# Performance work log

Measured on AMD Instinct MI355X. Metric: run time of the kernel, lower is better.

Reference implementation:

```python
import jax, jax.numpy as jnp
import numpy as np

D_MODEL = 1024
D_INNER = 2048
N_EXPERTS = 8
TOP_K = 2
INIT_STD = 0.02


def setup_inputs() -> dict:
    key = jax.random.key(0)
    ks = jax.random.split(key, 6)
    B, S = 2, 2048
    x = jax.random.normal(ks[0], (B, S, D_MODEL), dtype=jnp.float32)
    router_w = jax.random.normal(ks[1], (N_EXPERTS, D_MODEL), dtype=jnp.float32) * (INIT_STD * 0.1)
    router_b = jnp.zeros((N_EXPERTS,), dtype=jnp.float32)
    gate_w = jax.random.normal(ks[2], (N_EXPERTS, D_MODEL, D_INNER), dtype=jnp.float32) * INIT_STD
    up_w = jax.random.normal(ks[3], (N_EXPERTS, D_MODEL, D_INNER), dtype=jnp.float32) * INIT_STD
    down_w = jax.random.normal(ks[4], (N_EXPERTS, D_INNER, D_MODEL), dtype=jnp.float32) * INIT_STD
    return {"x": x, "router_w": router_w, "router_b": router_b,
            "gate_w": gate_w, "up_w": up_w, "down_w": down_w}


def reference(x, router_w, router_b, gate_w, up_w, down_w):
    # Router: softmax over experts, top-k, renormalize top-k probs.
    logits = jnp.einsum('bsd,ed->bse', x, router_w) + router_b          # [B,S,E]
    probs = jax.nn.softmax(logits, axis=-1)
    top_p, top_i = jax.lax.top_k(probs, TOP_K)                           # [B,S,K]
    top_p = top_p / jnp.sum(top_p, axis=-1, keepdims=True)
    # Per-expert combine weight: c[b,s,e] = sum_k top_p[b,s,k] * [top_i[b,s,k]==e]
    onehot = jax.nn.one_hot(top_i, N_EXPERTS, dtype=x.dtype)             # [B,S,K,E]
    combine = jnp.einsum('bsk,bske->bse', top_p, onehot)                 # [B,S,E]
    # SwiGLU FFN for every expert (dense form of the masked dispatch),
    # zeroed/weighted by combine coefficients.
    g = jnp.einsum('bsd,edf->ebsf', x, gate_w)                           # [E,B,S,F]
    u = jnp.einsum('bsd,edf->ebsf', x, up_w)
    h = jax.nn.silu(g) * u
    y = jnp.einsum('ebsf,efd->ebsd', h, down_w)                          # [E,B,S,D]
    out = jnp.einsum('ebsd,bse->bsd', y, combine)
    return out
```

## Files before the change

kernel.cpp:

```cpp
#include <hip/hip_runtime.h>
#include <hip/hip_bf16.h>
#include <stdint.h>

#define D_MODEL 1024
#define D_INNER 2048
#define NEXP 8
#define TOPK 2
#define T256 40
#define T128 72

typedef float f32x4 __attribute__((ext_vector_type(4)));
typedef short bf16x8 __attribute__((ext_vector_type(8)));

#define MEMFENCE asm volatile("" ::: "memory")

__device__ __forceinline__ unsigned short f2b(float f) {
    union { float f; uint32_t u; } v; v.f = f;
    uint32_t u = v.u;
    return (unsigned short)((u + 0x7fffu + ((u >> 16) & 1u)) >> 16);
}

__device__ __forceinline__ void gl_lds16(const void* g, void* l) {
    __builtin_amdgcn_global_load_lds((const __attribute__((address_space(1))) void*)g,
                                     (__attribute__((address_space(3))) void*)l, 16, 0, 0);
}

__global__ __launch_bounds__(256) void tcast3_kernel(
    const float* __restrict__ gw, const float* __restrict__ uw, const float* __restrict__ dw,
    unsigned short* __restrict__ gT, unsigned short* __restrict__ uT, unsigned short* __restrict__ dT)
{
    __shared__ unsigned short S[64][68];
    int which = blockIdx.z >> 3;
    int e = blockIdx.z & 7;
    const float* in; unsigned short* out; int K, N;
    if (which == 0)      { in = gw; out = gT; K = D_MODEL; N = D_INNER; }
    else if (which == 1) { in = uw; out = uT; K = D_MODEL; N = D_INNER; }
    else                 { in = dw; out = dT; K = D_INNER; N = D_MODEL; }
    int n0 = blockIdx.x * 64, k0 = blockIdx.y * 64;
    if (n0 >= N || k0 >= K) return;
    const float* ib = in + (size_t)e * K * N;
    unsigned short* ob = out + (size_t)e * N * K;
    int tid = threadIdx.x;
    int kk = tid >> 4, nn4 = (tid & 15) * 4;
#pragma unroll
    for (int j = 0; j < 4; j++) {
        int k = kk + 16 * j;
        float4 v = *(const float4*)&ib[(size_t)(k0 + k) * N + n0 + nn4];
        ushort4 s; s.x = f2b(v.x); s.y = f2b(v.y); s.z = f2b(v.z); s.w = f2b(v.w);
        *(ushort4*)&S[k][nn4] = s;
    }
    __syncthreads();
    int nn = tid >> 4, kk4 = (tid & 15) * 4;
#pragma unroll
    for (int j = 0; j < 4; j++) {
        int n = nn + 16 * j;
        ushort4 s;
        s.x = S[kk4 + 0][n]; s.y = S[kk4 + 1][n];
        s.z = S[kk4 + 2][n]; s.w = S[kk4 + 3][n];
        *(ushort4*)&ob[(size_t)(n0 + n) * K + k0 + kk4] = s;
    }
}

__global__ __launch_bounds__(64) void router_kernel(
    const float* __restrict__ x, const float* __restrict__ rw,
    const float* __restrict__ rb, unsigned short* __restrict__ xb,
    int* __restrict__ top_i, float* __restrict__ top_w, int T)
{
    int t = blockIdx.x;
    if (t >= T) return;
    int l = threadIdx.x;
    float xv[16];
#pragma unroll
    for (int i = 0; i < 16; i++) xv[i] = x[(size_t)t * D_MODEL + l + 64 * i];
#pragma unroll
    for (int i = 0; i < 16; i++) xb[(size_t)t * D_MODEL + l + 64 * i] = f2b(xv[i]);
    float logit[NEXP];
#pragma unroll
    for (int e = 0; e < NEXP; e++) {
        float acc = 0.f;
#pragma unroll
        for (int i = 0; i < 16; i++) acc += xv[i] * rw[e * D_MODEL + l + 64 * i];
#pragma unroll
        for (int s = 32; s > 0; s >>= 1) acc += __shfl_xor(acc, s, 64);
        logit[e] = acc + rb[e];
    }
    if (l == 0) {
        int i0 = 0; float m0 = logit[0];
#pragma unroll
        for (int e = 1; e < NEXP; e++) if (logit[e] > m0) { m0 = logit[e]; i0 = e; }
        int i1 = -1; float m1 = -3.0e38f;
#pragma unroll
        for (int e = 0; e < NEXP; e++) {
            if (e == i0) continue;
            if (logit[e] > m1) { m1 = logit[e]; i1 = e; }
        }
        float w0 = 1.f / (1.f + expf(m1 - m0));
        top_i[t * 2 + 0] = i0; top_i[t * 2 + 1] = i1;
        top_w[t * 2 + 0] = w0; top_w[t * 2 + 1] = 1.f - w0;
    }
}

__global__ __launch_bounds__(256) void bucket_kernel(
    const int* __restrict__ top_i, const float* __restrict__ top_w,
    int* __restrict__ meta, int* __restrict__ tok_of_slot,
    float* __restrict__ w_of_slot, int T)
{
    __shared__ int cnt[256][NEXP];
    __shared__ int pre[256][NEXP];
    __shared__ int tot[NEXP];
    __shared__ int off[NEXP + 1];
    int tid = threadIdx.x;
    int per = (T + 255) / 256;
    int t0 = tid * per;
    for (int e = 0; e < NEXP; e++) cnt[tid][e] = 0;
    for (int t = t0; t < t0 + per && t < T; t++)
        for (int k = 0; k < TOPK; k++) cnt[tid][top_i[t * 2 + k]]++;
    __syncthreads();
    if (tid < NEXP) {
        int run = 0;
        for (int i = 0; i < 256; i++) { pre[i][tid] = run; run += cnt[i][tid]; }
        tot[tid] = run;
    }
    __syncthreads();
    if (tid == 0) {
        off[0] = 0;
        for (int e = 0; e < NEXP; e++) off[e + 1] = off[e] + tot[e];
        for (int e = 0; e <= NEXP; e++) meta[e] = off[e];
        int nt = 0;
        for (int e = 0; e < NEXP; e++)
            for (int r = off[e]; r < off[e + 1]; r += 256)
                meta[16 + nt++] = (e << 16) | r;
        for (; nt < T256; nt++) meta[16 + nt] = -1;
        nt = 0;
        for (int e = 0; e < NEXP; e++)
            for (int r = off[e]; r < off[e + 1]; r += 128)
                meta[64 + nt++] = (e << 16) | r;
        for (; nt < T128; nt++) meta[64 + nt] = -1;
    }
    __syncthreads();
    int lc[NEXP];
#pragma unroll
    for (int e = 0; e < NEXP; e++) lc[e] = 0;
    for (int t = t0; t < t0 + per && t < T; t++) {
        for (int k = 0; k < TOPK; k++) {
            int e = top_i[t * 2 + k];
            int slot = off[e] + pre[tid][e] + lc[e]++;
            tok_of_slot[slot] = t;
            w_of_slot[slot] = top_w[t * 2 + k];
        }
    }
}

__global__ __launch_bounds__(512, 2) void moe_gate_up(
    const unsigned short* __restrict__ xb, const unsigned short* __restrict__ wgT,
    const unsigned short* __restrict__ wuT, const int* __restrict__ meta,
    const int* __restrict__ tok_of_slot, unsigned short* __restrict__ H)
{
    extern __shared__ __align__(16) unsigned short lds[];

    int lin = blockIdx.x;
    int strip = (lin & 7) * 2 + ((lin >> 3) & 1);
    int tix = lin >> 4;
    int packed = meta[16 + tix];
    if (packed < 0) return;
    int e = packed >> 16, row0 = packed & 0xffff;
    int Mloc = min(256, meta[e + 1] - row0);
    int f0 = strip * 128;

    int tid = threadIdx.x, wv = tid >> 6, lane = tid & 63;
    int c = tid & 7, rr = tid >> 3;

    const unsigned short* srcA[4];
    const unsigned short* srcG[2];
    const unsigned short* srcU[2];
#pragma unroll
    for (int j = 0; j < 4; j++) {
        int row = j * 64 + rr;
        int slot = row0 + ((row < Mloc) ? row : 0);
        srcA[j] = xb + (size_t)tok_of_slot[slot] * D_MODEL + 8 * (c ^ (row & 7));
    }
#pragma unroll
    for (int j = 0; j < 2; j++) {
        int row = j * 64 + rr;
        size_t wb = (size_t)e * D_MODEL * D_INNER + (size_t)(f0 + row) * D_MODEL + 8 * (c ^ (row & 7));
        srcG[j] = wgT + wb; srcU[j] = wuT + wb;
    }

    int wm = wv >> 1, wn = wv & 1;
    int lrow = lane & 15, kgrp = lane >> 4;
    int sw = lrow & 7;
    int co0 = 8 * (kgrp ^ sw);
    int co1 = 8 * ((4 + kgrp) ^ sw);

    int arow[4], brow[4];
#pragma unroll
    for (int i = 0; i < 4; i++) arow[i] = (wm * 64 + i * 16 + lrow) * 64;
#pragma unroll
    for (int i = 0; i < 4; i++) brow[i] = (wn * 64 + i * 16 + lrow) * 64;

    f32x4 accg[4][4], accu[4][4];
#pragma unroll
    for (int i = 0; i < 4; i++)
#pragma unroll
        for (int j = 0; j < 4; j++) {
            accg[i][j] = (f32x4){0.f, 0.f, 0.f, 0.f};
            accu[i][j] = (f32x4){0.f, 0.f, 0.f, 0.f};
        }

    auto stage = [&](int u) {
        int kk = u * 64;
        unsigned short* base = lds + (u & 1) * 32768;
#pragma unroll
        for (int j = 0; j < 4; j++)
            gl_lds16(srcA[j] + kk, base + (j * 512 + wv * 64) * 8);
#pragma unroll
        for (int j = 0; j < 2; j++) {
            gl_lds16(srcG[j] + kk, base + 16384 + (j * 512 + wv * 64) * 8);
            gl_lds16(srcU[j] + kk, base + 24576 + (j * 512 + wv * 64) * 8);
        }
    };

    bf16x8 a[4], bg[4], bu[4];
    auto load_frags = [&](int u, int co) {
        const unsigned short* base = lds + (u & 1) * 32768;
#pragma unroll
        for (int i = 0; i < 4; i++) a[i] = *(const bf16x8*)(base + arow[i] + co);
#pragma unroll
        for (int i = 0; i < 4; i++) bg[i] = *(const bf16x8*)(base + 16384 + brow[i] + co);
#pragma unroll
        for (int i = 0; i < 4; i++) bu[i] = *(const bf16x8*)(base + 24576 + brow[i] + co);
    };

    const int NT = D_MODEL / 64;
    stage(0);
    MEMFENCE;
    asm volatile("s_waitcnt vmcnt(0)" ::: "memory");
    __builtin_amdgcn_s_barrier();
    MEMFENCE;
    load_frags(0, co0);

    for (int t = 0; t < NT; ++t) {
        if (t + 1 < NT) stage(t + 1);
        __builtin_amdgcn_sched_barrier(0);
        __builtin_amdgcn_s_setprio(1);
#pragma unroll
        for (int fm = 0; fm < 4; fm++)
#pragma unroll
            for (int fn = 0; fn < 4; fn++) {
                accg[fm][fn] = __builtin_amdgcn_mfma_f32_16x16x32_bf16(a[fm], bg[fn], accg[fm][fn], 0, 0, 0);
                accu[fm][fn] = __builtin_amdgcn_mfma_f32_16x16x32_bf16(a[fm], bu[fn], accu[fm][fn], 0, 0, 0);
            }
        __builtin_amdgcn_s_setprio(0);
        load_frags(t, co1);
        __builtin_amdgcn_s_setprio(1);
#pragma unroll
        for (int fm = 0; fm < 4; fm++)
#pragma unroll
            for (int fn = 0; fn < 4; fn++) {
                accg[fm][fn] = __builtin_amdgcn_mfma_f32_16x16x32_bf16(a[fm], bg[fn], accg[fm][fn], 0, 0, 0);
                accu[fm][fn] = __builtin_amdgcn_mfma_f32_16x16x32_bf16(a[fm], bu[fn], accu[fm][fn], 0, 0, 0);
            }
        __builtin_amdgcn_s_setprio(0);
        __builtin_amdgcn_sched_barrier(0);
        asm volatile("s_waitcnt vmcnt(0)" ::: "memory");
        __builtin_amdgcn_s_barrier();
        MEMFENCE;
        if (t + 1 < NT) load_frags(t + 1, co0);
    }

#pragma unroll
    for (int fm = 0; fm < 4; fm++)
#pragma unroll
        for (int fn = 0; fn < 4; fn++)
#pragma unroll
            for (int r = 0; r < 4; r++) {
                int m = wm * 64 + fm * 16 + kgrp * 4 + r;
                if (m < Mloc) {
                    int n = wn * 64 + fn * 16 + lrow;
                    float g = accg[fm][fn][r], u = accu[fm][fn][r];
                    float h = g / (1.f + __expf(-g)) * u;
                    H[(size_t)(row0 + m) * D_INNER + f0 + n] = f2b(h);
                }
            }
}

__global__ __launch_bounds__(512, 2) void moe_down(
    const unsigned short* __restrict__ H, const unsigned short* __restrict__ wdT,
    const int* __restrict__ meta, const int* __restrict__ tok_of_slot,
    const float* __restrict__ w_of_slot, float* __restrict__ out, int S2)
{
    extern __shared__ __align__(16) unsigned short lds[];
    __shared__ int toks[128];
    __shared__ float wts[128];

    int lin = blockIdx.x;
    int d0 = (lin & 3) * 256;
    int tix = lin >> 2;
    int packed = meta[64 + tix];
    if (packed < 0) return;
    int e = packed >> 16, row0 = packed & 0xffff;
    int Mloc = min(128, meta[e + 1] - row0);

    int tid = threadIdx.x, wv = tid >> 6, lane = tid & 63;
    if (tid < 128) {
        bool v = tid < Mloc;
        toks[tid] = v ? tok_of_slot[row0 + tid] : 0;
        wts[tid] = v ? w_of_slot[row0 + tid] : 0.f;
    }
    int c = tid & 7, rr = tid >> 3;

    const unsigned short* srcA[2];
    const unsigned short* srcB[4];
#pragma unroll
    for (int j = 0; j < 2; j++) {
        int row = j * 64 + rr;
        int slot = min(row0 + row, S2 - 1);
        srcA[j] = H + (size_t)slot * D_INNER + 8 * (c ^ (row & 7));
    }
#pragma unroll
    for (int j = 0; j < 4; j++) {
        int row = j * 64 + rr;
        srcB[j] = wdT + (size_t)e * D_INNER * D_MODEL + (size_t)(d0 + row) * D_INNER + 8 * (c ^ (row & 7));
    }

    int wm = wv >> 2, wn = wv & 3;
    int lrow = lane & 15, kgrp = lane >> 4;
    int sw = lrow & 7;
    int co0 = 8 * (kgrp ^ sw);
    int co1 = 8 * ((4 + kgrp) ^ sw);

    int arow[4], brow[4];
#pragma unroll
    for (int i = 0; i < 4; i++) arow[i] = (wm * 64 + i * 16 + lrow) * 64;
#pragma unroll
    for (int i = 0; i < 4; i++) brow[i] = 8192 + (wn * 64 + i * 16 + lrow) * 64;

    f32x4 acc[4][4];
#pragma unroll
    for (int i = 0; i < 4; i++)
#pragma unroll
        for (int j = 0; j < 4; j++) acc[i][j] = (f32x4){0.f, 0.f, 0.f, 0.f};

    auto stage = [&](int u) {
        int kk = u * 64;
        unsigned short* base = lds + (u & 1) * 24576;
#pragma unroll
        for (int j = 0; j < 2; j++)
            gl_lds16(srcA[j] + kk, base + (j * 512 + wv * 64) * 8);
#pragma unroll
        for (int j = 0; j < 4; j++)
            gl_lds16(srcB[j] + kk, base + 8192 + (j * 512 + wv * 64) * 8);
    };

    bf16x8 a[4], b[4];
    auto load_frags = [&](int u, int co) {
        const unsigned short* base = lds + (u & 1) * 24576;
#pragma unroll
        for (int i = 0; i < 4; i++) a[i] = *(const bf16x8*)(base + arow[i] + co);
#pragma unroll
        for (int i = 0; i < 4; i++) b[i] = *(const bf16x8*)(base + brow[i] + co);
    };

    const int NT = D_INNER / 64;
    stage(0);
    MEMFENCE;
    asm volatile("s_waitcnt vmcnt(0)" ::: "memory");
    __builtin_amdgcn_s_barrier();
    MEMFENCE;
    load_frags(0, co0);

    for (int t = 0; t < NT; ++t) {
        if (t + 1 < NT) stage(t + 1);
        __builtin_amdgcn_sched_barrier(0);
        __builtin_amdgcn_s_setprio(1);
#pragma unroll
        for (int fm = 0; fm < 4; fm++)
#pragma unroll
            for (int fn = 0; fn < 4; fn++)
                acc[fm][fn] = __builtin_amdgcn_mfma_f32_16x16x32_bf16(a[fm], b[fn], acc[fm][fn], 0, 0, 0);
        __builtin_amdgcn_s_setprio(0);
        load_frags(t, co1);
        __builtin_amdgcn_s_setprio(1);
#pragma unroll
        for (int fm = 0; fm < 4; fm++)
#pragma unroll
            for (int fn = 0; fn < 4; fn++)
                acc[fm][fn] = __builtin_amdgcn_mfma_f32_16x16x32_bf16(a[fm], b[fn], acc[fm][fn], 0, 0, 0);
        __builtin_amdgcn_s_setprio(0);
        __builtin_amdgcn_sched_barrier(0);
        asm volatile("s_waitcnt vmcnt(0)" ::: "memory");
        __builtin_amdgcn_s_barrier();
        MEMFENCE;
        if (t + 1 < NT) load_frags(t + 1, co0);
    }

#pragma unroll
    for (int fm = 0; fm < 4; fm++)
#pragma unroll
        for (int fn = 0; fn < 4; fn++)
#pragma unroll
            for (int r = 0; r < 4; r++) {
                int m = wm * 64 + fm * 16 + kgrp * 4 + r;
                if (m < Mloc) {
                    int n = wn * 64 + fn * 16 + lrow;
                    atomicAdd(&out[(size_t)toks[m] * D_MODEL + d0 + n], wts[m] * acc[fm][fn][r]);
                }
            }
}

extern "C" void kernel_launch(void* const* d_in, const int* in_sizes, int n_in,
                              void* d_out, int out_size, void* d_ws, size_t ws_size,
                              hipStream_t stream) {
    const float* x  = (const float*)d_in[0];
    const float* rw = (const float*)d_in[1];
    const float* rb = (const float*)d_in[2];
    const float* gw = (const float*)d_in[3];
    const float* uw = (const float*)d_in[4];
    const float* dw = (const float*)d_in[5];
    float* out = (float*)d_out;

    int T = in_sizes[0] / D_MODEL;
    int S2 = 2 * T;

    char* ws = (char*)d_ws;
    size_t cur = 0;
    auto take = [&](size_t bytes) { char* p = ws + cur; cur = (cur + bytes + 255) & ~(size_t)255; return p; };
    int*   top_i = (int*)take((size_t)S2 * 4);
    float* top_w = (float*)take((size_t)S2 * 4);
    int*   meta  = (int*)take(1024);
    int*   tos   = (int*)take((size_t)S2 * 4);
    float* wos   = (float*)take((size_t)S2 * 4);
    unsigned short* xb  = (unsigned short*)take((size_t)T * D_MODEL * 2);
    unsigned short* wgT = (unsigned short*)take((size_t)NEXP * D_MODEL * D_INNER * 2);
    unsigned short* wuT = (unsigned short*)take((size_t)NEXP * D_MODEL * D_INNER * 2);
    unsigned short* wdT = (unsigned short*)take((size_t)NEXP * D_MODEL * D_INNER * 2);
    unsigned short* H   = (unsigned short*)take((size_t)S2 * D_INNER * 2);

    static const int GU_LDS = 2 * 32768 * 2;
    static const int DN_LDS = 2 * 24576 * 2;
    hipFuncSetAttribute((const void*)moe_gate_up,
                        hipFuncAttributeMaxDynamicSharedMemorySize, GU_LDS);
    hipFuncSetAttribute((const void*)moe_down,
                        hipFuncAttributeMaxDynamicSharedMemorySize, DN_LDS);

    hipMemsetAsync(d_out, 0, (size_t)out_size * sizeof(float), stream);

    tcast3_kernel<<<dim3(32, 32, 24), 256, 0, stream>>>(gw, uw, dw, wgT, wuT, wdT);
    router_kernel<<<T, 64, 0, stream>>>(x, rw, rb, xb, top_i, top_w, T);
    bucket_kernel<<<1, 256, 0, stream>>>(top_i, top_w, meta, tos, wos, T);

    moe_gate_up<<<T256 * 16, 512, GU_LDS, stream>>>(xb, wgT, wuT, meta, tos, H);
    moe_down<<<T128 * 4, 512, DN_LDS, stream>>>(H, wdT, meta, tos, wos, out, S2);
}
```

Before: 269.8 us.

## Shrink MoE GEMM tiles to 128-row blocks with 3-stage LDS ring pipeline

Both expert GEMM kernels move from 512-thread blocks with 256x128 or 128x256 tiles and a double-buffered 64-wide K step to 256-thread blocks with 128x64 or 128x128 tiles, a 32-wide K step and a triple-buffered LDS ring that keeps two stages in flight via partial vmcnt waits. In gate/up, separate waves now compute gate and up, and the SwiGLU is combined through an LDS exchange. The intent is more blocks and more resident blocks per CU, plus better overlap of global loads, on a grid that is otherwise small and imbalanced. In exchange, each tile reuses data less, so global traffic per FLOP rises, and there are more barriers per unit of K.

```diff
diff --git a/kernel.cpp b/kernel.cpp
--- a/kernel.cpp
+++ b/kernel.cpp
@@ -13,6 +13,12 @@
 typedef short bf16x8 __attribute__((ext_vector_type(8)));
 
 #define MEMFENCE asm volatile("" ::: "memory")
+#define SB __builtin_amdgcn_sched_barrier(0)
+#define LGKM0 asm volatile("s_waitcnt lgkmcnt(0)" ::: "memory")
+#define VM0 asm volatile("s_waitcnt vmcnt(0)" ::: "memory")
+#define VM4 asm volatile("s_waitcnt vmcnt(4)" ::: "memory")
+#define BAR __builtin_amdgcn_s_barrier()
+#define SW2(r) (((r) >> 1) & 3)
 
 __device__ __forceinline__ unsigned short f2b(float f) {
     union { float f; uint32_t u; } v; v.f = f;
@@ -130,11 +136,13 @@
         for (int e = 0; e < NEXP; e++)
             for (int r = off[e]; r < off[e + 1]; r += 256)
                 meta[16 + nt++] = (e << 16) | r;
+        meta[11] = nt;
         for (; nt < T256; nt++) meta[16 + nt] = -1;
         nt = 0;
         for (int e = 0; e < NEXP; e++)
             for (int r = off[e]; r < off[e + 1]; r += 128)
                 meta[64 + nt++] = (e << 16) | r;
+        meta[12] = nt;
         for (; nt < T128; nt++) meta[64 + nt] = -1;
     }
     __syncthreads();
@@ -151,7 +159,7 @@
     }
 }
 
-__global__ __launch_bounds__(512, 2) void moe_gate_up(
+__global__ __launch_bounds__(256, 3) void moe_gate_up(
     const unsigned short* __restrict__ xb, const unsigned short* __restrict__ wgT,
     const unsigned short* __restrict__ wuT, const int* __restrict__ meta,
     const int* __restrict__ tok_of_slot, unsigned short* __restrict__ H)
@@ -159,132 +167,125 @@
     extern __shared__ __align__(16) unsigned short lds[];
 
     int lin = blockIdx.x;
-    int strip = (lin & 7) * 2 + ((lin >> 3) & 1);
-    int tix = lin >> 4;
-    int packed = meta[16 + tix];
+    int strip = (lin & 7) * 4 + ((lin >> 3) & 3);
+    int tix = lin >> 5;
+    int packed = meta[64 + tix];
     if (packed < 0) return;
     int e = packed >> 16, row0 = packed & 0xffff;
-    int Mloc = min(256, meta[e + 1] - row0);
-    int f0 = strip * 128;
+    int Mloc = min(128, meta[e + 1] - row0);
+    int f0 = strip * 64;
 
     int tid = threadIdx.x, wv = tid >> 6, lane = tid & 63;
-    int c = tid & 7, rr = tid >> 3;
-
-    const unsigned short* srcA[4];
-    const unsigned short* srcG[2];
-    const unsigned short* srcU[2];
-#pragma unroll
-    for (int j = 0; j < 4; j++) {
-        int row = j * 64 + rr;
-        int slot = row0 + ((row < Mloc) ? row : 0);
-        srcA[j] = xb + (size_t)tok_of_slot[slot] * D_MODEL + 8 * (c ^ (row & 7));
-    }
+    int lrow = lane & 15, kgrp = lane >> 4;
+    int sel = wv & 1, wm = wv >> 1;
+    int co = 8 * (kgrp ^ SW2(lrow));
+
+    const unsigned short* sA[2];
+    int dA[2];
 #pragma unroll
     for (int j = 0; j < 2; j++) {
-        int row = j * 64 + rr;
-        size_t wb = (size_t)e * D_MODEL * D_INNER + (size_t)(f0 + row) * D_MODEL + 8 * (c ^ (row & 7));
-        srcG[j] = wgT + wb; srcU[j] = wuT + wb;
-    }
-
-    int wm = wv >> 1, wn = wv & 1;
-    int lrow = lane & 15, kgrp = lane >> 4;
-    int sw = lrow & 7;
-    int co0 = 8 * (kgrp ^ sw);
-    int co1 = 8 * ((4 + kgrp) ^ sw);
-
-    int arow[4], brow[4];
-#pragma unroll
-    for (int i = 0; i < 4; i++) arow[i] = (wm * 64 + i * 16 + lrow) * 64;
-#pragma unroll
-    for (int i = 0; i < 4; i++) brow[i] = (wn * 64 + i * 16 + lrow) * 64;
-
-    f32x4 accg[4][4], accu[4][4];
+        int idx = j * 256 + tid;
+        int r = idx >> 2, c = idx & 3;
+        int slot = row0 + ((r < Mloc) ? r : 0);
+        sA[j] = xb + (size_t)tok_of_slot[slot] * D_MODEL + 8 * (c ^ SW2(r));
+        dA[j] = idx * 8;
+    }
+    const unsigned short *sG, *sU;
+    {
+        int r = tid >> 2, c = tid & 3;
+        size_t wb = (size_t)e * D_MODEL * D_INNER + (size_t)(f0 + r) * D_MODEL + 8 * (c ^ SW2(r));
+        sG = wgT + wb; sU = wuT + wb;
+    }
+
+    int aoff[4], boff[4];
+#pragma unroll
+    for (int i = 0; i < 4; i++) aoff[i] = (wm * 64 + i * 16 + lrow) * 32 + co;
+    int bb = sel ? 6144 : 4096;
+#pragma unroll
+    for (int i = 0; i < 4; i++) boff[i] = bb + (i * 16 + lrow) * 32 + co;
+
+    f32x4 acc[4][4];
 #pragma unroll
     for (int i = 0; i < 4; i++)
 #pragma unroll
-        for (int j = 0; j < 4; j++) {
-            accg[i][j] = (f32x4){0.f, 0.f, 0.f, 0.f};
-            accu[i][j] = (f32x4){0.f, 0.f, 0.f, 0.f};
-        }
+        for (int j = 0; j < 4; j++) acc[i][j] = (f32x4){0.f, 0.f, 0.f, 0.f};
 
     auto stage = [&](int u) {
-        int kk = u * 64;
-        unsigned short* base = lds + (u & 1) * 32768;
-#pragma unroll
-        for (int j = 0; j < 4; j++)
-            gl_lds16(srcA[j] + kk, base + (j * 512 + wv * 64) * 8);
-#pragma unroll
-        for (int j = 0; j < 2; j++) {
-            gl_lds16(srcG[j] + kk, base + 16384 + (j * 512 + wv * 64) * 8);
-            gl_lds16(srcU[j] + kk, base + 24576 + (j * 512 + wv * 64) * 8);
-        }
+        int kk = u * 32;
+        unsigned short* b = lds + (u % 3) * 8192;
+        gl_lds16(sA[0] + kk, b + dA[0]);
+        gl_lds16(sA[1] + kk, b + dA[1]);
+        gl_lds16(sG + kk, b + 4096 + tid * 8);
+        gl_lds16(sU + kk, b + 6144 + tid * 8);
     };
 
-    bf16x8 a[4], bg[4], bu[4];
-    auto load_frags = [&](int u, int co) {
-        const unsigned short* base = lds + (u & 1) * 32768;
-#pragma unroll
-        for (int i = 0; i < 4; i++) a[i] = *(const bf16x8*)(base + arow[i] + co);
-#pragma unroll
-        for (int i = 0; i < 4; i++) bg[i] = *(const bf16x8*)(base + 16384 + brow[i] + co);
-#pragma unroll
-        for (int i = 0; i < 4; i++) bu[i] = *(const bf16x8*)(base + 24576 + brow[i] + co);
+    bf16x8 a[4], bfr[4];
+    auto load_frags = [&](int u) {
+        const unsigned short* b = lds + (u % 3) * 8192;
+#pragma unroll
+        for (int i = 0; i < 4; i++) a[i] = *(const bf16x8*)(b + aoff[i]);
+#pragma unroll
+        for (int i = 0; i < 4; i++) bfr[i] = *(const bf16x8*)(b + boff[i]);
     };
 
-    const int NT = D_MODEL / 64;
-    stage(0);
+    const int NT = D_MODEL / 32;
+    stage(0); stage(1);
     MEMFENCE;
-    asm volatile("s_waitcnt vmcnt(0)" ::: "memory");
-    __builtin_amdgcn_s_barrier();
-    MEMFENCE;
-    load_frags(0, co0);
+    VM4;
+    BAR; MEMFENCE;
+    load_frags(0);
 
     for (int t = 0; t < NT; ++t) {
-        if (t + 1 < NT) stage(t + 1);
-        __builtin_amdgcn_sched_barrier(0);
+        if (t + 2 < NT) stage(t + 2);
+        SB;
         __builtin_amdgcn_s_setprio(1);
 #pragma unroll
-        for (int fm = 0; fm < 4; fm++)
-#pragma unroll
-            for (int fn = 0; fn < 4; fn++) {
-                accg[fm][fn] = __builtin_amdgcn_mfma_f32_16x16x32_bf16(a[fm], bg[fn], accg[fm][fn], 0, 0, 0);
-                accu[fm][fn] = __builtin_amdgcn_mfma_f32_16x16x32_bf16(a[fm], bu[fn], accu[fm][fn], 0, 0, 0);
-            }
+        for (int i = 0; i < 4; i++)
+#pragma unroll
+            for (int j = 0; j < 4; j++)
+                acc[i][j] = __builtin_amdgcn_mfma_f32_16x16x32_bf16(a[i], bfr[j], acc[i][j], 0, 0, 0);
         __builtin_amdgcn_s_setprio(0);
-        load_frags(t, co1);
-        __builtin_amdgcn_s_setprio(1);
-#pragma unroll
-        for (int fm = 0; fm < 4; fm++)
-#pragma unroll
-            for (int fn = 0; fn < 4; fn++) {
-                accg[fm][fn] = __builtin_amdgcn_mfma_f32_16x16x32_bf16(a[fm], bg[fn], accg[fm][fn], 0, 0, 0);
-                accu[fm][fn] = __builtin_amdgcn_mfma_f32_16x16x32_bf16(a[fm], bu[fn], accu[fm][fn], 0, 0, 0);
-            }
-        __builtin_amdgcn_s_setprio(0);
-        __builtin_amdgcn_sched_barrier(0);
-        asm volatile("s_waitcnt vmcnt(0)" ::: "memory");
-        __builtin_amdgcn_s_barrier();
-        MEMFENCE;
-        if (t + 1 < NT) load_frags(t + 1, co0);
-    }
-
-#pragma unroll
-    for (int fm = 0; fm < 4; fm++)
-#pragma unroll
-        for (int fn = 0; fn < 4; fn++)
-#pragma unroll
-            for (int r = 0; r < 4; r++) {
-                int m = wm * 64 + fm * 16 + kgrp * 4 + r;
-                if (m < Mloc) {
-                    int n = wn * 64 + fn * 16 + lrow;
-                    float g = accg[fm][fn][r], u = accu[fm][fn][r];
-                    float h = g / (1.f + __expf(-g)) * u;
-                    H[(size_t)(row0 + m) * D_INNER + f0 + n] = f2b(h);
+        SB;
+        LGKM0;
+        if (t + 2 < NT) { VM4; } else { VM0; }
+        BAR; MEMFENCE;
+        if (t + 1 < NT) load_frags(t + 1);
+    }
+
+    __syncthreads();
+    float* ex = (float*)lds;
+    if (sel == 1) {
+        float* dst = ex + wm * 4160;
+#pragma unroll
+        for (int i = 0; i < 4; i++)
+#pragma unroll
+            for (int j = 0; j < 4; j++)
+#pragma unroll
+                for (int r = 0; r < 4; r++)
+                    dst[(i * 16 + kgrp * 4 + r) * 65 + j * 16 + lrow] = acc[i][j][r];
+    }
+    __syncthreads();
+    if (sel == 0) {
+        const float* src = ex + wm * 4160;
+#pragma unroll
+        for (int i = 0; i < 4; i++)
+#pragma unroll
+            for (int j = 0; j < 4; j++)
+#pragma unroll
+                for (int r = 0; r < 4; r++) {
+                    int row = i * 16 + kgrp * 4 + r;
+                    int m = wm * 64 + row;
+                    if (m < Mloc) {
+                        float g = acc[i][j][r];
+                        float u = src[row * 65 + j * 16 + lrow];
+                        float h = g / (1.f + __expf(-g)) * u;
+                        H[(size_t)(row0 + m) * D_INNER + f0 + j * 16 + lrow] = f2b(h);
+                    }
                 }
-            }
-}
-
-__global__ __launch_bounds__(512, 2) void moe_down(
+    }
+}
+
+__global__ __launch_bounds__(256, 3) void moe_down(
     const unsigned short* __restrict__ H, const unsigned short* __restrict__ wdT,
     const int* __restrict__ meta, const int* __restrict__ tok_of_slot,
     const float* __restrict__ w_of_slot, float* __restrict__ out, int S2)
@@ -294,46 +295,42 @@
     __shared__ float wts[128];
 
     int lin = blockIdx.x;
-    int d0 = (lin & 3) * 256;
-    int tix = lin >> 2;
+    int d0 = (lin & 7) * 128;
+    int tix = lin >> 3;
     int packed = meta[64 + tix];
     if (packed < 0) return;
     int e = packed >> 16, row0 = packed & 0xffff;
     int Mloc = min(128, meta[e + 1] - row0);
 
     int tid = threadIdx.x, wv = tid >> 6, lane = tid & 63;
+    int lrow = lane & 15, kgrp = lane >> 4;
+    int wn = wv & 1, wm = wv >> 1;
+    int co = 8 * (kgrp ^ SW2(lrow));
+
     if (tid < 128) {
         bool v = tid < Mloc;
         toks[tid] = v ? tok_of_slot[row0 + tid] : 0;
         wts[tid] = v ? w_of_slot[row0 + tid] : 0.f;
     }
-    int c = tid & 7, rr = tid >> 3;
-
-    const unsigned short* srcA[2];
-    const unsigned short* srcB[4];
+
+    const unsigned short* sA[2];
+    const unsigned short* sB[2];
+    int dA[2];
 #pragma unroll
     for (int j = 0; j < 2; j++) {
-        int row = j * 64 + rr;
-        int slot = min(row0 + row, S2 - 1);
-        srcA[j] = H + (size_t)slot * D_INNER + 8 * (c ^ (row & 7));
-    }
-#pragma unroll
-    for (int j = 0; j < 4; j++) {
-        int row = j * 64 + rr;
-        srcB[j] = wdT + (size_t)e * D_INNER * D_MODEL + (size_t)(d0 + row) * D_INNER + 8 * (c ^ (row & 7));
-    }
-
-    int wm = wv >> 2, wn = wv & 3;
-    int lrow = lane & 15, kgrp = lane >> 4;
-    int sw = lrow & 7;
-    int co0 = 8 * (kgrp ^ sw);
-    int co1 = 8 * ((4 + kgrp) ^ sw);
-
-    int arow[4], brow[4];
-#pragma unroll
-    for (int i = 0; i < 4; i++) arow[i] = (wm * 64 + i * 16 + lrow) * 64;
-#pragma unroll
-    for (int i = 0; i < 4; i++) brow[i] = 8192 + (wn * 64 + i * 16 + lrow) * 64;
+        int idx = j * 256 + tid;
+        int r = idx >> 2, c = idx & 3;
+        int slot = min(row0 + r, S2 - 1);
+        sA[j] = H + (size_t)slot * D_INNER + 8 * (c ^ SW2(r));
+        sB[j] = wdT + (size_t)e * D_INNER * D_MODEL + (size_t)(d0 + r) * D_INNER + 8 * (c ^ SW2(r));
+        dA[j] = idx * 8;
+    }
+
+    int aoff[4], boff[4];
+#pragma unroll
+    for (int i = 0; i < 4; i++) aoff[i] = (wm * 64 + i * 16 + lrow) * 32 + co;
+#pragma unroll
+    for (int i = 0; i < 4; i++) boff[i] = 4096 + (wn * 64 + i * 16 + lrow) * 32 + co;
 
     f32x4 acc[4][4];
 #pragma unroll
@@ -342,68 +339,57 @@
         for (int j = 0; j < 4; j++) acc[i][j] = (f32x4){0.f, 0.f, 0.f, 0.f};
 
     auto stage = [&](int u) {
-        int kk = u * 64;
-        unsigned short* base = lds + (u & 1) * 24576;
-#pragma unroll
-        for (int j = 0; j < 2; j++)
-            gl_lds16(srcA[j] + kk, base + (j * 512 + wv * 64) * 8);
+        int kk = u * 32;
+        unsigned short* b = lds + (u % 3) * 8192;
+        gl_lds16(sA[0] + kk, b + dA[0]);
+        gl_lds16(sA[1] + kk, b + dA[1]);
+        gl_lds16(sB[0] + kk, b + 4096 + dA[0]);
+        gl_lds16(sB[1] + kk, b + 4096 + dA[1]);
+    };
+
+    bf16x8 a[4], bfr[4];
+    auto load_frags = [&](int u) {
+        const unsigned short* b = lds + (u % 3) * 8192;
+#pragma unroll
+        for (int i = 0; i < 4; i++) a[i] = *(const bf16x8*)(b + aoff[i]);
+#pragma unroll
+        for (int i = 0; i < 4; i++) bfr[i] = *(const bf16x8*)(b + boff[i]);
+    };
+
+    const int NT = D_INNER / 32;
+    stage(0); stage(1);
+    MEMFENCE;
+    VM4;
+    BAR; MEMFENCE;
+    load_frags(0);
+
+    for (int t = 0; t < NT; ++t) {
+        if (t + 2 < NT) stage(t + 2);
+        SB;
+        __builtin_amdgcn_s_setprio(1);
+#pragma unroll
+        for (int i = 0; i < 4; i++)
+#pragma unroll
+            for (int j = 0; j < 4; j++)
+                acc[i][j] = __builtin_amdgcn_mfma_f32_16x16x32_bf16(a[i], bfr[j], acc[i][j], 0, 0, 0);
+        __builtin_amdgcn_s_setprio(0);
+        SB;
+        LGKM0;
+        if (t + 2 < NT) { VM4; } else { VM0; }
+        BAR; MEMFENCE;
+        if (t + 1 < NT) load_frags(t + 1);
+    }
+
+#pragma unroll
+    for (int i = 0; i < 4; i++)
 #pragma unroll
         for (int j = 0; j < 4; j++)
-            gl_lds16(srcB[j] + kk, base + 8192 + (j * 512 + wv * 64) * 8);
-    };
-
-    bf16x8 a[4], b[4];
-    auto load_frags = [&](int u, int co) {
-        const unsigned short* base = lds + (u & 1) * 24576;
-#pragma unroll
-        for (int i = 0; i < 4; i++) a[i] = *(const bf16x8*)(base + arow[i] + co);
-#pragma unroll
-        for (int i = 0; i < 4; i++) b[i] = *(const bf16x8*)(base + brow[i] + co);
-    };
-
-    const int NT = D_INNER / 64;
-    stage(0);
-    MEMFENCE;
-    asm volatile("s_waitcnt vmcnt(0)" ::: "memory");
-    __builtin_amdgcn_s_barrier();
-    MEMFENCE;
-    load_frags(0, co0);
-
-    for (int t = 0; t < NT; ++t) {
-        if (t + 1 < NT) stage(t + 1);
-        __builtin_amdgcn_sched_barrier(0);
-        __builtin_amdgcn_s_setprio(1);
-#pragma unroll
-        for (int fm = 0; fm < 4; fm++)
-#pragma unroll
-            for (int fn = 0; fn < 4; fn++)
-                acc[fm][fn] = __builtin_amdgcn_mfma_f32_16x16x32_bf16(a[fm], b[fn], acc[fm][fn], 0, 0, 0);
-        __builtin_amdgcn_s_setprio(0);
-        load_frags(t, co1);
-        __builtin_amdgcn_s_setprio(1);
-#pragma unroll
-        for (int fm = 0; fm < 4; fm++)
-#pragma unroll
-            for (int fn = 0; fn < 4; fn++)
-                acc[fm][fn] = __builtin_amdgcn_mfma_f32_16x16x32_bf16(a[fm], b[fn], acc[fm][fn], 0, 0, 0);
-        __builtin_amdgcn_s_setprio(0);
-        __builtin_amdgcn_sched_barrier(0);
-        asm volatile("s_waitcnt vmcnt(0)" ::: "memory");
-        __builtin_amdgcn_s_barrier();
-        MEMFENCE;
-        if (t + 1 < NT) load_frags(t + 1, co0);
-    }
-
-#pragma unroll
-    for (int fm = 0; fm < 4; fm++)
-#pragma unroll
-        for (int fn = 0; fn < 4; fn++)
 #pragma unroll
             for (int r = 0; r < 4; r++) {
-                int m = wm * 64 + fm * 16 + kgrp * 4 + r;
+                int m = wm * 64 + i * 16 + kgrp * 4 + r;
                 if (m < Mloc) {
-                    int n = wn * 64 + fn * 16 + lrow;
-                    atomicAdd(&out[(size_t)toks[m] * D_MODEL + d0 + n], wts[m] * acc[fm][fn][r]);
+                    int n = d0 + wn * 64 + j * 16 + lrow;
+                    atomicAdd(&out[(size_t)toks[m] * D_MODEL + n], wts[m] * acc[i][j][r]);
                 }
             }
 }
@@ -436,12 +422,11 @@
     unsigned short* wdT = (unsigned short*)take((size_t)NEXP * D_MODEL * D_INNER * 2);
     unsigned short* H   = (unsigned short*)take((size_t)S2 * D_INNER * 2);
 
-    static const int GU_LDS = 2 * 32768 * 2;
-    static const int DN_LDS = 2 * 24576 * 2;
+    static const int RING_LDS = 3 * 8192 * 2;
     hipFuncSetAttribute((const void*)moe_gate_up,
-                        hipFuncAttributeMaxDynamicSharedMemorySize, GU_LDS);
+                        hipFuncAttributeMaxDynamicSharedMemorySize, RING_LDS);
     hipFuncSetAttribute((const void*)moe_down,
-                        hipFuncAttributeMaxDynamicSharedMemorySize, DN_LDS);
+                        hipFuncAttributeMaxDynamicSharedMemorySize, RING_LDS);
 
     hipMemsetAsync(d_out, 0, (size_t)out_size * sizeof(float), stream);
 
@@ -449,6 +434,6 @@
     router_kernel<<<T, 64, 0, stream>>>(x, rw, rb, xb, top_i, top_w, T);
     bucket_kernel<<<1, 256, 0, stream>>>(top_i, top_w, meta, tos, wos, T);
 
-    moe_gate_up<<<T256 * 16, 512, GU_LDS, stream>>>(xb, wgT, wuT, meta, tos, H);
-    moe_down<<<T128 * 4, 512, DN_LDS, stream>>>(H, wdT, meta, tos, wos, out, S2);
-}
+    moe_gate_up<<<T128 * 32, 256, RING_LDS, stream>>>(xb, wgT, wuT, meta, tos, H);
+    moe_down<<<T128 * 8, 256, RING_LDS, stream>>>(H, wdT, meta, tos, wos, out, S2);
+}
```

Result: no change. 272.1 us (+0.9%).
